# Kernel tuning notes

Hardware: AMD Instinct MI355X
Metric: run time of the kernel (lower is better)

The kernel has to match this reference:

```python
import jax, jax.numpy as jnp
import numpy as np

EPS = 1e-6
OMEGA = 0.1


def setup_inputs() -> dict:
    key = jax.random.key(0)
    k1, k2 = jax.random.split(key)
    n, d, kk = 4096, 128, 4
    inputs = jax.random.uniform(k1, (n, d), dtype=jnp.float32)  # positive so log(sim) is finite
    labels = jax.random.randint(k2, (n, kk), 0, 64, dtype=jnp.int64)
    return {"inputs": inputs, "labels": labels}


def reference(inputs, labels):
    n, kk = labels.shape
    sim = inputs @ inputs.T                      # [n, n]
    logsim = jnp.log(sim + EPS)                  # a_{jk} = log(sim[j,k]+eps)
    targets = labels[:, 0]
    eye = jnp.eye(n, dtype=bool)
    # pos_mask[j,k] = (targets[j] == targets[k]) xor diagonal
    pos = (targets[:, None] == targets[None, :]) & ~eye
    # eq[j,l,i] = (labels[l,i] == targets[j])
    eq = targets[:, None, None] == labels[None, :, :]
    m_idx = jnp.arange(kk)
    cols = kk - 1 - m_idx                        # neg_mask[m] uses label column kk-1-m
    # neg_mask[m][j,l] == 1  <=>  ~eq[j,l,kk-1-m]  AND  (m==0 or eq[j,l,kk-m])
    neq_col = ~eq[:, :, cols]                    # [j,l,m]
    prev_ok = jnp.concatenate(
        [jnp.ones((n, n, 1), dtype=bool), eq[:, :, cols[:-1]]], axis=-1)
    neg = neq_col & prev_ok                      # [j,l,m]
    # loss_pair[m] = log(Omega+eps) - log(Omega^(kk-m+1)+eps)
    lp = jnp.log(OMEGA + EPS) - jnp.log(OMEGA ** (kk - m_idx + 1) + EPS)  # [kk]
    dt = logsim.dtype
    posf = pos.astype(dt)
    negf = neg.astype(dt)
    # term = (a_jk - b_jlm)^2 with b_jlm = logsim[j,l] + 0.1*lp[m]
    # expand: sum_jklm pos*neg*(a^2 - 2ab + b^2), separable over k and (l,m)
    c = posf.sum(1)                              # [j] count of positives
    S1 = (posf * logsim).sum(1)                  # [j] sum a
    S2 = (posf * logsim ** 2).sum(1)             # [j] sum a^2
    b = logsim[:, :, None] + 0.1 * lp[None, None, :]   # [j,l,m]
    Ncnt = negf.sum(1)                           # [j,m]
    T1 = (negf * b).sum(1)                       # [j,m]
    T2 = (negf * b ** 2).sum(1)                  # [j,m]
    loss = (S2[:, None] * Ncnt - 2.0 * S1[:, None] * T1 + c[:, None] * T2).sum()
    return loss
```

## Files before the change

### kernel.cpp

```cpp
#include <hip/hip_runtime.h>
#include <math.h>

constexpr int N  = 4096;
constexpr int D  = 128;
constexpr int NT = 64;

constexpr size_t TAB_OFF = 0;
constexpr size_t XBF_OFF = (size_t)4 << 20;
constexpr size_t ACC_OFF = (size_t)5 << 20;
constexpr size_t LSD_OFF = ((size_t)5 << 20) + ((size_t)96 << 10);

typedef __attribute__((ext_vector_type(8))) short short8;
typedef __attribute__((ext_vector_type(4))) float floatx4;
typedef __attribute__((address_space(1))) unsigned int gu32;
typedef __attribute__((address_space(3))) unsigned int lu32;

__device__ inline unsigned f2bf(float f) {
  unsigned u = __builtin_bit_cast(unsigned, f);
  return (u + 0x7FFFu + ((u >> 16) & 1u)) >> 16;
}

__global__ __launch_bounds__(256) void k1_prep(
    const float* __restrict__ X, const int* __restrict__ labels,
    char* __restrict__ ws, float* __restrict__ out,
    float B0, float B1, float B2, float B3,
    float Q0, float Q1, float Q2, float Q3) {
  const int b = blockIdx.x, t = threadIdx.x;
  if (b < 1024) {
    const int idx = b * 256 + t;
    const int tt = idx >> 12;
    const int j  = idx & (N - 1);
    const int4 L = ((const int4*)labels)[j];
    const bool e0 = (tt == L.x), e1 = (tt == L.y), e2 = (tt == L.z), e3 = (tt == L.w);
    const bool n0 = !e3, n1 = e3 && !e2, n2 = e2 && !e1, n3 = e1 && !e0;
    const float g0 = (float)((n0 ? 1 : 0) + (n1 ? 1 : 0) + (n2 ? 1 : 0) + (n3 ? 1 : 0));
    const float gB = (n0 ? B0 : 0.f) + (n1 ? B1 : 0.f) + (n2 ? B2 : 0.f) + (n3 ? B3 : 0.f);
    const float gQ = (n0 ? Q0 : 0.f) + (n1 ? Q1 : 0.f) + (n2 ? Q2 : 0.f) + (n3 ? Q3 : 0.f);
    ((float4*)(ws + TAB_OFF))[idx] = make_float4(gB, gQ, g0, e0 ? 1.f : 0.f);
    if (idx < 6 * N) ((float*)(ws + ACC_OFF))[idx] = 0.f;
  } else if (b < 1280) {
    const int task = (b - 1024) * 256 + t;
    const int r   = task >> 4;
    const int blk = task & 15;
    const float4 x0 = *(const float4*)&X[r * D + blk * 8];
    const float4 x1 = *(const float4*)&X[r * D + blk * 8 + 4];
    uint4 wv;
    wv.x = f2bf(x0.x) | (f2bf(x0.y) << 16);
    wv.y = f2bf(x0.z) | (f2bf(x0.w) << 16);
    wv.z = f2bf(x1.x) | (f2bf(x1.y) << 16);
    wv.w = f2bf(x1.z) | (f2bf(x1.w) << 16);
    *(uint4*)(ws + XBF_OFF + (size_t)r * 256 + ((blk ^ (r & 15)) * 16)) = wv;
  } else {
    const int i = (b - 1280) * 256 + t;
    const float* xr = X + i * D;
    float s = 0.f;
#pragma unroll
    for (int c = 0; c < 32; ++c) {
      const float4 v = ((const float4*)xr)[c];
      s += v.x * v.x + v.y * v.y + v.z * v.z + v.w * v.w;
    }
    ((float*)(ws + LSD_OFF))[i] = __logf(s + 1e-6f);
    if (b == 1295 && t == 0) out[0] = 0.f;
  }
}

__global__ __launch_bounds__(512, 4) void logratio_phaseA(
    const char* __restrict__ ws_ro, const int* __restrict__ labels,
    float* acc6) {

  __shared__ __align__(16) char smem[65536];

  const int tid  = threadIdx.x;
  const int w    = tid >> 6;
  const int lane = tid & 63;
  const int lc   = lane & 15;
  const int quad = lane >> 4;
  const int jBase = blockIdx.x * 128;
  const int iBase = blockIdx.y * 128;

  const char* xbf = ws_ro + XBF_OFF;
  const char* gB_ = xbf + (size_t)jBase * 256 + w * 4096 + lane * 16;
  const char* gA_ = xbf + (size_t)iBase * 256 + w * 4096 + lane * 16;
#pragma unroll
  for (int c = 0; c < 4; ++c) {
    __builtin_amdgcn_global_load_lds((const gu32*)(gB_ + c * 1024),
                                     (lu32*)(smem + w * 4096 + c * 1024), 16, 0, 0);
    __builtin_amdgcn_global_load_lds((const gu32*)(gA_ + c * 1024),
                                     (lu32*)(smem + 32768 + w * 4096 + c * 1024), 16, 0, 0);
  }

  int tis[4];
#pragma unroll
  for (int reg = 0; reg < 4; ++reg)
    tis[reg] = labels[(iBase + w * 16 + quad * 4 + reg) * 4];

  __syncthreads();

  floatx4 acc[8] = {};
  const char* Abase = smem + 32768 + (w * 16 + lc) * 256;
#pragma unroll
  for (int kb = 0; kb < 4; ++kb) {
    const int pb = ((kb * 4 + quad) ^ lc) * 16;
    const short8 af = *(const short8*)(Abase + pb);
    short8 bfr[8];
#pragma unroll
    for (int tn = 0; tn < 8; ++tn)
      bfr[tn] = *(const short8*)(smem + (tn * 16 + lc) * 256 + pb);
#pragma unroll
    for (int tn = 0; tn < 8; ++tn)
      acc[tn] = __builtin_amdgcn_mfma_f32_16x16x32_bf16(af, bfr[tn], acc[tn], 0, 0, 0);
  }

  __syncthreads();
  float* Red = (float*)smem;

  const float4* tab = (const float4*)(ws_ro + TAB_OFF);
#pragma unroll
  for (int reg = 0; reg < 4; ++reg) {
    const int row = w * 16 + quad * 4 + reg;
    const float4* trow = tab + (size_t)tis[reg] * N + jBase + lc;

    float a_c = 0.f, a_s1 = 0.f, a_s2 = 0.f;
    float a_A = 0.f, a_B = 0.f, a_C = 0.f;
#pragma unroll
    for (int tn = 0; tn < 8; ++tn) {
      const float4 cf = trow[tn * 16];
      const float ls = __logf(acc[tn][reg] + 1e-6f);
      const float t1 = fmaf(cf.z, ls, cf.x);
      a_A += cf.z;
      a_B += t1;
      a_C += fmaf(t1 + cf.x, ls, cf.y);
      const float fls = cf.w * ls;
      a_c += cf.w;
      a_s1 += fls;
      a_s2 = fmaf(fls, ls, a_s2);
    }
    float* dst = Red + row * 97 + lc * 6;
    dst[0] = a_c;  dst[1] = a_s1; dst[2] = a_s2;
    dst[3] = a_A;  dst[4] = a_B;  dst[5] = a_C;
  }
  __syncthreads();

  if (tid < 128) {
    const int gi = iBase + tid;
    const float* src = Red + tid * 97;
    float s0 = 0.f, s1 = 0.f, s2 = 0.f, s3 = 0.f, s4 = 0.f, s5 = 0.f;
#pragma unroll
    for (int l = 0; l < 16; ++l) {
      s0 += src[l * 6 + 0]; s1 += src[l * 6 + 1]; s2 += src[l * 6 + 2];
      s3 += src[l * 6 + 3]; s4 += src[l * 6 + 4]; s5 += src[l * 6 + 5];
    }
    atomicAdd(&acc6[0 * N + gi], s0);
    atomicAdd(&acc6[1 * N + gi], s1);
    atomicAdd(&acc6[2 * N + gi], s2);
    atomicAdd(&acc6[3 * N + gi], s3);
    atomicAdd(&acc6[4 * N + gi], s4);
    atomicAdd(&acc6[5 * N + gi], s5);
  }
}

__global__ __launch_bounds__(256) void logratio_phaseB(
    const char* __restrict__ ws_ro, float* out) {
  const int i = blockIdx.x * 256 + threadIdx.x;
  const float* acc6 = (const float*)(ws_ro + ACC_OFF);
  float c  = acc6[0 * N + i];
  float S1 = acc6[1 * N + i];
  float S2 = acc6[2 * N + i];
  const float A = acc6[3 * N + i];
  const float B = acc6[4 * N + i];
  const float C = acc6[5 * N + i];
  const float lsd = ((const float*)(ws_ro + LSD_OFF))[i];
  c  -= 1.f;
  S1 -= lsd;
  S2 -= lsd * lsd;
  float v = S2 * A - 2.f * S1 * B + c * C;
#pragma unroll
  for (int m = 32; m >= 1; m >>= 1) v += __shfl_xor(v, m, 64);
  __shared__ float wsum[4];
  if ((threadIdx.x & 63) == 0) wsum[threadIdx.x >> 6] = v;
  __syncthreads();
  if (threadIdx.x == 0) atomicAdd(out, wsum[0] + wsum[1] + wsum[2] + wsum[3]);
}

extern "C" void kernel_launch(void* const* d_in, const int* in_sizes, int n_in,
                              void* d_out, int out_size, void* d_ws, size_t ws_size,
                              hipStream_t stream) {
  const float* inputs = (const float*)d_in[0];
  const int* labels = (const int*)d_in[1];
  float* out = (float*)d_out;
  char* ws = (char*)d_ws;

  float Bq[4], Qq[4];
  for (int m = 0; m < 4; ++m) {
    const float lpv = logf(0.1f + 1e-6f) - logf(powf(0.1f, (float)(5 - m)) + 1e-6f);
    Bq[m] = 0.1f * lpv;
    Qq[m] = Bq[m] * Bq[m];
  }

  k1_prep<<<1296, 256, 0, stream>>>(inputs, labels, ws, out,
                                    Bq[0], Bq[1], Bq[2], Bq[3],
                                    Qq[0], Qq[1], Qq[2], Qq[3]);
  dim3 grid(N / 128, N / 128);
  logratio_phaseA<<<grid, 512, 0, stream>>>(ws, labels, (float*)(ws + ACC_OFF));
  logratio_phaseB<<<N / 256, 256, 0, stream>>>(ws, out);
}
```

Baseline: 83.91 us.

## Replace dense per-target coefficient table with sparse per-block label-match lists

Phase A no longer reads a dense 16-byte coefficient per (target, column). The reduction is rewritten as dense row sums of log-sim and log-sim squared, plus sparse corrections. Those corrections come from per-(target, 128-column block) lists of columns whose labels match the target, built in prep with atomics. Log-sims are staged transposed in LDS and the listed columns are gathered from there. Per-target constant sums are folded in during phase B. This removes heavy table traffic at the cost of an extra zeroing launch and a fixed 64-entry list cap, which silently drops matches if a block ever has more than 64.

New measurement: 97.37 us. 1.16x slower.

```diff
diff --git a/kernel.cpp b/kernel.cpp
--- a/kernel.cpp
+++ b/kernel.cpp
@@ -1,14 +1,15 @@
 #include <hip/hip_runtime.h>
 #include <math.h>
 
-constexpr int N  = 4096;
-constexpr int D  = 128;
-constexpr int NT = 64;
-
-constexpr size_t TAB_OFF = 0;
-constexpr size_t XBF_OFF = (size_t)4 << 20;
-constexpr size_t ACC_OFF = (size_t)5 << 20;
-constexpr size_t LSD_OFF = ((size_t)5 << 20) + ((size_t)96 << 10);
+constexpr int N = 4096;
+constexpr int D = 128;
+
+constexpr size_t XBF_OFF = 0;
+constexpr size_t ACC_OFF = (size_t)1 << 20;
+constexpr size_t LSD_OFF = ACC_OFF + 7 * 4096 * 4;
+constexpr size_t CNT_OFF = LSD_OFF + 4096 * 4;
+constexpr size_t LST_OFF = CNT_OFF + 64 * 32 * 4;
+constexpr size_t SUM_OFF = LST_OFF + 64 * 32 * 64 * 2;
 
 typedef __attribute__((ext_vector_type(8))) short short8;
 typedef __attribute__((ext_vector_type(4))) float floatx4;
@@ -20,26 +21,57 @@
   return (u + 0x7FFFu + ((u >> 16) & 1u)) >> 16;
 }
 
+__global__ __launch_bounds__(256) void k0_zero(char* __restrict__ ws, float* __restrict__ out) {
+  const int idx = blockIdx.x * 256 + threadIdx.x;
+  if (idx < 7 * 4096) ((float*)(ws + ACC_OFF))[idx] = 0.f;
+  else ((unsigned*)(ws + CNT_OFF))[idx - 7 * 4096] = 0u;
+  if (idx == 0) out[0] = 0.f;
+}
+
 __global__ __launch_bounds__(256) void k1_prep(
-    const float* __restrict__ X, const int* __restrict__ labels,
-    char* __restrict__ ws, float* __restrict__ out,
+    const float* __restrict__ X, const int* __restrict__ labels, char* __restrict__ ws,
     float B0, float B1, float B2, float B3,
     float Q0, float Q1, float Q2, float Q3) {
-  const int b = blockIdx.x, t = threadIdx.x;
-  if (b < 1024) {
-    const int idx = b * 256 + t;
-    const int tt = idx >> 12;
-    const int j  = idx & (N - 1);
-    const int4 L = ((const int4*)labels)[j];
-    const bool e0 = (tt == L.x), e1 = (tt == L.y), e2 = (tt == L.z), e3 = (tt == L.w);
-    const bool n0 = !e3, n1 = e3 && !e2, n2 = e2 && !e1, n3 = e1 && !e0;
-    const float g0 = (float)((n0 ? 1 : 0) + (n1 ? 1 : 0) + (n2 ? 1 : 0) + (n3 ? 1 : 0));
-    const float gB = (n0 ? B0 : 0.f) + (n1 ? B1 : 0.f) + (n2 ? B2 : 0.f) + (n3 ? B3 : 0.f);
-    const float gQ = (n0 ? Q0 : 0.f) + (n1 ? Q1 : 0.f) + (n2 ? Q2 : 0.f) + (n3 ? Q3 : 0.f);
-    ((float4*)(ws + TAB_OFF))[idx] = make_float4(gB, gQ, g0, e0 ? 1.f : 0.f);
-    if (idx < 6 * N) ((float*)(ws + ACC_OFF))[idx] = 0.f;
-  } else if (b < 1280) {
-    const int task = (b - 1024) * 256 + t;
+  __shared__ float red[4][4];
+  const int b = blockIdx.x, tid = threadIdx.x;
+  if (b < 64) {
+    const int t = b;
+    unsigned* cnt = (unsigned*)(ws + CNT_OFF);
+    unsigned short* lst = (unsigned short*)(ws + LST_OFF);
+    float sg0 = 0.f, sgB = 0.f, sgQ = 0.f, ce0 = 0.f;
+    for (int j = tid; j < N; j += 256) {
+      const int4 L = ((const int4*)labels)[j];
+      const bool e0 = (t == L.x), e1 = (t == L.y), e2 = (t == L.z), e3 = (t == L.w);
+      const bool n1 = e3 && !e2, n2 = e2 && !e1, n3 = e1 && !e0;
+      sg0 += (e3 ? 0.f : 1.f) + (n1 ? 1.f : 0.f) + (n2 ? 1.f : 0.f) + (n3 ? 1.f : 0.f);
+      sgB += (e3 ? 0.f : B0) + (n1 ? B1 : 0.f) + (n2 ? B2 : 0.f) + (n3 ? B3 : 0.f);
+      sgQ += (e3 ? 0.f : Q0) + (n1 ? Q1 : 0.f) + (n2 ? Q2 : 0.f) + (n3 ? Q3 : 0.f);
+      ce0 += e0 ? 1.f : 0.f;
+      const unsigned m = (e0 ? 1u : 0u) | (e1 ? 2u : 0u) | (e2 ? 4u : 0u) | (e3 ? 8u : 0u);
+      if (m) {
+        const int jb = j >> 7;
+        const unsigned slot = atomicAdd(&cnt[t * 32 + jb], 1u);
+        if (slot < 64u)
+          lst[(t * 32 + jb) * 64 + slot] = (unsigned short)(((j & 127) << 4) | m);
+      }
+    }
+    const int w = tid >> 6, lane = tid & 63;
+#pragma unroll
+    for (int s = 1; s <= 32; s <<= 1) {
+      sg0 += __shfl_xor(sg0, s, 64); sgB += __shfl_xor(sgB, s, 64);
+      sgQ += __shfl_xor(sgQ, s, 64); ce0 += __shfl_xor(ce0, s, 64);
+    }
+    if (lane == 0) { red[w][0] = sg0; red[w][1] = sgB; red[w][2] = sgQ; red[w][3] = ce0; }
+    __syncthreads();
+    if (tid == 0) {
+      float* sums = (float*)(ws + SUM_OFF);
+      sums[t * 4 + 0] = red[0][0] + red[1][0] + red[2][0] + red[3][0];
+      sums[t * 4 + 1] = red[0][1] + red[1][1] + red[2][1] + red[3][1];
+      sums[t * 4 + 2] = red[0][2] + red[1][2] + red[2][2] + red[3][2];
+      sums[t * 4 + 3] = red[0][3] + red[1][3] + red[2][3] + red[3][3];
+    }
+  } else if (b < 320) {
+    const int task = (b - 64) * 256 + tid;
     const int r   = task >> 4;
     const int blk = task & 15;
     const float4 x0 = *(const float4*)&X[r * D + blk * 8];
@@ -51,7 +83,7 @@
     wv.w = f2bf(x1.z) | (f2bf(x1.w) << 16);
     *(uint4*)(ws + XBF_OFF + (size_t)r * 256 + ((blk ^ (r & 15)) * 16)) = wv;
   } else {
-    const int i = (b - 1280) * 256 + t;
+    const int i = (b - 320) * 256 + tid;
     const float* xr = X + i * D;
     float s = 0.f;
 #pragma unroll
@@ -60,15 +92,14 @@
       s += v.x * v.x + v.y * v.y + v.z * v.z + v.w * v.w;
     }
     ((float*)(ws + LSD_OFF))[i] = __logf(s + 1e-6f);
-    if (b == 1295 && t == 0) out[0] = 0.f;
   }
 }
 
 __global__ __launch_bounds__(512, 4) void logratio_phaseA(
     const char* __restrict__ ws_ro, const int* __restrict__ labels,
-    float* acc6) {
-
-  __shared__ __align__(16) char smem[65536];
+    float* acc7, float B0, float B1, float B2, float B3) {
+
+  __shared__ __align__(16) char smem[66560];
 
   const int tid  = threadIdx.x;
   const int w    = tid >> 6;
@@ -88,12 +119,6 @@
     __builtin_amdgcn_global_load_lds((const gu32*)(gA_ + c * 1024),
                                      (lu32*)(smem + 32768 + w * 4096 + c * 1024), 16, 0, 0);
   }
-
-  int tis[4];
-#pragma unroll
-  for (int reg = 0; reg < 4; ++reg)
-    tis[reg] = labels[(iBase + w * 16 + quad * 4 + reg) * 4];
-
   __syncthreads();
 
   floatx4 acc[8] = {};
@@ -110,70 +135,96 @@
     for (int tn = 0; tn < 8; ++tn)
       acc[tn] = __builtin_amdgcn_mfma_f32_16x16x32_bf16(af, bfr[tn], acc[tn], 0, 0, 0);
   }
-
-  __syncthreads();
-  float* Red = (float*)smem;
-
-  const float4* tab = (const float4*)(ws_ro + TAB_OFF);
+  __syncthreads();
+
+  float* lsT   = (float*)smem;
+  float* rowTT = (float*)(smem + 65536);
+
+  const int r0 = w * 16 + quad * 4;
+  float T0r[4] = {0.f, 0.f, 0.f, 0.f};
+  float T1r[4] = {0.f, 0.f, 0.f, 0.f};
+#pragma unroll
+  for (int tn = 0; tn < 8; ++tn) {
+    const int col = tn * 16 + lc;
+    floatx4 lsv;
+#pragma unroll
+    for (int reg = 0; reg < 4; ++reg) {
+      const float ls = __logf(acc[tn][reg] + 1e-6f);
+      lsv[reg] = ls;
+      T0r[reg] += ls;
+      T1r[reg] = fmaf(ls, ls, T1r[reg]);
+    }
+    *(floatx4*)(lsT + col * 128 + (r0 ^ ((col & 7) << 2))) = lsv;
+  }
 #pragma unroll
   for (int reg = 0; reg < 4; ++reg) {
-    const int row = w * 16 + quad * 4 + reg;
-    const float4* trow = tab + (size_t)tis[reg] * N + jBase + lc;
-
-    float a_c = 0.f, a_s1 = 0.f, a_s2 = 0.f;
-    float a_A = 0.f, a_B = 0.f, a_C = 0.f;
-#pragma unroll
-    for (int tn = 0; tn < 8; ++tn) {
-      const float4 cf = trow[tn * 16];
-      const float ls = __logf(acc[tn][reg] + 1e-6f);
-      const float t1 = fmaf(cf.z, ls, cf.x);
-      a_A += cf.z;
-      a_B += t1;
-      a_C += fmaf(t1 + cf.x, ls, cf.y);
-      const float fls = cf.w * ls;
-      a_c += cf.w;
-      a_s1 += fls;
-      a_s2 = fmaf(fls, ls, a_s2);
-    }
-    float* dst = Red + row * 97 + lc * 6;
-    dst[0] = a_c;  dst[1] = a_s1; dst[2] = a_s2;
-    dst[3] = a_A;  dst[4] = a_B;  dst[5] = a_C;
+    float t0 = T0r[reg], t1 = T1r[reg];
+#pragma unroll
+    for (int s = 1; s <= 8; s <<= 1) {
+      t0 += __shfl_xor(t0, s, 64);
+      t1 += __shfl_xor(t1, s, 64);
+    }
+    if (lc == 0) {
+      rowTT[(r0 + reg) * 2]     = t0;
+      rowTT[(r0 + reg) * 2 + 1] = t1;
+    }
   }
   __syncthreads();
 
   if (tid < 128) {
-    const int gi = iBase + tid;
-    const float* src = Red + tid * 97;
-    float s0 = 0.f, s1 = 0.f, s2 = 0.f, s3 = 0.f, s4 = 0.f, s5 = 0.f;
-#pragma unroll
-    for (int l = 0; l < 16; ++l) {
-      s0 += src[l * 6 + 0]; s1 += src[l * 6 + 1]; s2 += src[l * 6 + 2];
-      s3 += src[l * 6 + 3]; s4 += src[l * 6 + 4]; s5 += src[l * 6 + 5];
-    }
-    atomicAdd(&acc6[0 * N + gi], s0);
-    atomicAdd(&acc6[1 * N + gi], s1);
-    atomicAdd(&acc6[2 * N + gi], s2);
-    atomicAdd(&acc6[3 * N + gi], s3);
-    atomicAdd(&acc6[4 * N + gi], s4);
-    atomicAdd(&acc6[5 * N + gi], s5);
+    const int r = tid, gi = iBase + r;
+    const int t = labels[gi * 4];
+    const int jb = blockIdx.x;
+    const unsigned* cntA = (const unsigned*)(ws_ro + CNT_OFF);
+    const unsigned short* lst = (const unsigned short*)(ws_ro + LST_OFF) + (t * 32 + jb) * 64;
+    unsigned cnt = cntA[t * 32 + jb];
+    if (cnt > 64u) cnt = 64u;
+    float U0 = 0.f, U1 = 0.f, V = 0.f, P1 = 0.f, P2 = 0.f;
+    for (unsigned k = 0; k < cnt; ++k) {
+      const unsigned e = lst[k];
+      const int jl = (int)(e >> 4);
+      const unsigned m = e & 15u;
+      const float ls = lsT[jl * 128 + (r ^ ((jl & 7) << 2))];
+      const bool e0 = m & 1u, e1 = m & 2u, e2 = m & 4u, e3 = m & 8u;
+      const bool n1 = e3 && !e2, n2 = e2 && !e1, n3 = e1 && !e0;
+      const float dg0 = (e3 ? -1.f : 0.f) + (n1 ? 1.f : 0.f) + (n2 ? 1.f : 0.f) + (n3 ? 1.f : 0.f);
+      const float dgB = (e3 ? -B0 : 0.f) + (n1 ? B1 : 0.f) + (n2 ? B2 : 0.f) + (n3 ? B3 : 0.f);
+      const float e0f = e0 ? 1.f : 0.f;
+      U0 = fmaf(dg0, ls, U0);
+      U1 = fmaf(dg0 * ls, ls, U1);
+      V  = fmaf(dgB, ls, V);
+      P1 = fmaf(e0f, ls, P1);
+      P2 = fmaf(e0f * ls, ls, P2);
+    }
+    atomicAdd(&acc7[0 * N + gi], rowTT[r * 2]);
+    atomicAdd(&acc7[1 * N + gi], rowTT[r * 2 + 1]);
+    atomicAdd(&acc7[2 * N + gi], U0);
+    atomicAdd(&acc7[3 * N + gi], U1);
+    atomicAdd(&acc7[4 * N + gi], V);
+    atomicAdd(&acc7[5 * N + gi], P1);
+    atomicAdd(&acc7[6 * N + gi], P2);
   }
 }
 
 __global__ __launch_bounds__(256) void logratio_phaseB(
-    const char* __restrict__ ws_ro, float* out) {
+    const char* __restrict__ ws_ro, const int* __restrict__ labels,
+    float* out, float B0) {
   const int i = blockIdx.x * 256 + threadIdx.x;
-  const float* acc6 = (const float*)(ws_ro + ACC_OFF);
-  float c  = acc6[0 * N + i];
-  float S1 = acc6[1 * N + i];
-  float S2 = acc6[2 * N + i];
-  const float A = acc6[3 * N + i];
-  const float B = acc6[4 * N + i];
-  const float C = acc6[5 * N + i];
+  const float* acc7 = (const float*)(ws_ro + ACC_OFF);
+  const float T0 = acc7[0 * N + i], T1 = acc7[1 * N + i];
+  const float U0 = acc7[2 * N + i], U1 = acc7[3 * N + i];
+  const float V  = acc7[4 * N + i];
+  const float P1 = acc7[5 * N + i], P2 = acc7[6 * N + i];
+  const int t = labels[i * 4];
+  const float4 S = ((const float4*)(ws_ro + SUM_OFF))[t];
   const float lsd = ((const float*)(ws_ro + LSD_OFF))[i];
-  c  -= 1.f;
-  S1 -= lsd;
-  S2 -= lsd * lsd;
-  float v = S2 * A - 2.f * S1 * B + c * C;
+  const float c  = S.w - 1.f;
+  const float S1 = P1 - lsd;
+  const float S2 = P2 - lsd * lsd;
+  const float A  = S.x;
+  const float Bv = T0 + U0 + S.y;
+  const float Cv = T1 + U1 + 2.f * fmaf(B0, T0, V) + S.z;
+  float v = S2 * A - 2.f * S1 * Bv + c * Cv;
 #pragma unroll
   for (int m = 32; m >= 1; m >>= 1) v += __shfl_xor(v, m, 64);
   __shared__ float wsum[4];
@@ -197,10 +248,12 @@
     Qq[m] = Bq[m] * Bq[m];
   }
 
-  k1_prep<<<1296, 256, 0, stream>>>(inputs, labels, ws, out,
-                                    Bq[0], Bq[1], Bq[2], Bq[3],
-                                    Qq[0], Qq[1], Qq[2], Qq[3]);
+  k0_zero<<<120, 256, 0, stream>>>(ws, out);
+  k1_prep<<<336, 256, 0, stream>>>(inputs, labels, ws,
+                                   Bq[0], Bq[1], Bq[2], Bq[3],
+                                   Qq[0], Qq[1], Qq[2], Qq[3]);
   dim3 grid(N / 128, N / 128);
-  logratio_phaseA<<<grid, 512, 0, stream>>>(ws, labels, (float*)(ws + ACC_OFF));
-  logratio_phaseB<<<N / 256, 256, 0, stream>>>(ws, out);
-}
+  logratio_phaseA<<<grid, 512, 0, stream>>>(ws, labels, (float*)(ws + ACC_OFF),
+                                            Bq[0], Bq[1], Bq[2], Bq[3]);
+  logratio_phaseB<<<N / 256, 256, 0, stream>>>(ws, labels, out, Bq[0]);
+}
```
